# Optimization experiments

Hardware: AMD Instinct MI355X
Metric: run time of the kernel (lower is better)

The kernel has to match this reference:

```python
import jax, jax.numpy as jnp
import numpy as np

K = 20
EPS = 1e-5
N = 4096


def lrelu(x):
    return jnp.where(x >= 0, x, 0.2 * x)


def bn(x, g, b, m, v):
    # eval-mode BatchNorm over channel dim 1
    shape = [1] * x.ndim
    shape[1] = -1
    inv = g / jnp.sqrt(v + EPS)
    return (x - m.reshape(shape)) * inv.reshape(shape) + b.reshape(shape)


def get_graph_feature(x):
    # Faithful to repo: num_points = x.shape[1], remaining dims fold into channels.
    p = x.shape[1]
    x2d = x.reshape(-1, p)              # (C, P)
    xx = jnp.sum(x2d * x2d, axis=0)     # (P,)
    dist = 2.0 * (x2d.T @ x2d) - xx[:, None] - xx[None, :]  # -||xi-xj||^2, (P, P)
    idx = jax.lax.top_k(dist, K)[1]     # (P, K) nearest neighbors (incl. self)
    xt = x2d.T                          # (P, C)
    feat = xt[idx]                      # (P, K, C) neighbor gather
    ctr = jnp.broadcast_to(xt[:, None, :], feat.shape)
    out = jnp.concatenate([feat - ctr, ctr], axis=-1)  # (P, K, 2C)
    return out.transpose(2, 0, 1)[None]                # (1, 2C, P, K)


def setup_inputs():
    key = jax.random.key(0)
    ks = jax.random.split(key, 16)

    def w(k_, o, c):
        return jax.random.normal(k_, (o, c), jnp.float32) / float(np.sqrt(c))

    def bnp(k_, c):
        k1, k2, k3, k4 = jax.random.split(k_, 4)
        return (1.0 + 0.1 * jax.random.normal(k1, (c,), jnp.float32),
                0.1 * jax.random.normal(k2, (c,), jnp.float32),
                0.1 * jax.random.normal(k3, (c,), jnp.float32),
                jax.random.uniform(k4, (c,), jnp.float32, minval=0.5, maxval=1.5))

    g1, b1, m1, v1 = bnp(ks[1], 64)
    g2, b2, m2, v2 = bnp(ks[2], 64)
    g3, b3, m3, v3 = bnp(ks[3], 128)
    g4, b4, m4, v4 = bnp(ks[4], 256)
    g5, b5, m5, v5 = bnp(ks[5], 512)
    return dict(
        x=jax.random.normal(ks[0], (3, N), jnp.float32),
        w1=w(ks[6], 64, 6), g1=g1, b1=b1, m1=m1, v1=v1,
        w2=w(ks[7], 64, 64), g2=g2, b2=b2, m2=m2, v2=v2,
        w3=w(ks[8], 128, 64), g3=g3, b3=b3, m3=m3, v3=v3,
        w4=w(ks[9], 256, 128), g4=g4, b4=b4, m4=m4, v4=v4,
        w5=w(ks[10], 512, 256), g5=g5, b5=b5, m5=m5, v5=v5,
        lw1=w(ks[11], 512, 1024),
        lw2=w(ks[12], 256, 512),
        lb2=0.1 * jax.random.normal(ks[13], (256,), jnp.float32),
        ow=w(ks[14], 11, 256),
        ob=0.1 * jax.random.normal(ks[15], (11,), jnp.float32),
    )


def reference(x, w1, g1, b1, m1, v1, w2, g2, b2, m2, v2, w3, g3, b3, m3, v3,
              w4, g4, b4, m4, v4, w5, g5, b5, m5, v5, lw1, lw2, lb2, ow, ob):
    conv2d = lambda w_, f_: jnp.einsum('oc,bcpk->bopk', w_, f_)

    f = get_graph_feature(x)                                   # (1, 6, N, K)
    h = lrelu(bn(conv2d(w1, f), g1, b1, m1, v1))
    x1 = jnp.max(h, axis=-1)                                   # (1, 64, N)

    f = jnp.swapaxes(get_graph_feature(x1), 1, 2)              # (1, 64, 2N, K)
    h = lrelu(bn(conv2d(w2, f), g2, b2, m2, v2))
    x2 = jnp.max(h, axis=-1)                                   # (1, 64, 2N)

    f = jnp.swapaxes(get_graph_feature(x2), 1, 2)              # (1, 64, 4N, K)
    h = lrelu(bn(conv2d(w3, f), g3, b3, m3, v3))
    x3 = jnp.max(h, axis=-1)                                   # (1, 128, 4N)

    f = jnp.swapaxes(get_graph_feature(x3), 1, 2)              # (1, 128, 8N, K)
    h = lrelu(bn(conv2d(w4, f), g4, b4, m4, v4))
    x4 = jnp.max(h, axis=-1)                                   # (1, 256, 8N)

    h5 = lrelu(bn(jnp.einsum('oc,bcp->bop', w5, x4), g5, b5, m5, v5))  # (1, 512, 8N)
    pmax = jnp.max(h5, axis=-1)
    pavg = jnp.mean(h5, axis=-1)
    z = jnp.concatenate([pmax, pavg], axis=1)                  # (1, 1024)
    z = lrelu(z @ lw1.T)                                       # (1, 512); dropout = eval identity
    z = lrelu(z @ lw2.T + lb2)                                 # (1, 256)
    logits = z @ ow.T + ob                                     # (1, 11)
    return jax.nn.softmax(logits, axis=1)
```

## Files before the change

kernel.cpp:

```cpp
#include <hip/hip_runtime.h>
#include <hip/hip_bf16.h>
#include <float.h>
#include <math.h>

#define DEV __device__ __forceinline__

DEV float lrelu(float x) { return x >= 0.f ? x : 0.2f * x; }

constexpr int N = 4096, KNN = 20;

typedef __attribute__((ext_vector_type(4))) float f32x4;
typedef __attribute__((ext_vector_type(8))) short s16x8;

constexpr size_t OFF_SC1 = 0,    OFF_SH1 = 64;
constexpr size_t OFF_SC2 = 128,  OFF_SH2 = 192;
constexpr size_t OFF_SC3 = 256,  OFF_SH3 = 384;
constexpr size_t OFF_SC4 = 512,  OFF_SH4 = 768;
constexpr size_t OFF_SC5 = 1024, OFF_SH5 = 1536;
constexpr size_t OFF_X1 = 2048;
constexpr size_t OFF_X2 = OFF_X1 + (size_t)64*4096;
constexpr size_t OFF_X3 = OFF_X2 + (size_t)64*8192;
constexpr size_t OFF_X4 = OFF_X3 + (size_t)128*16384;
constexpr size_t OFF_A  = OFF_X4 + (size_t)256*32768;
constexpr size_t OFF_GP = OFF_A + (size_t)256*21*128;
constexpr size_t OFF_PM = OFF_GP + (size_t)64*128*128;
constexpr size_t OFF_PS = OFF_PM + (size_t)512*256;
constexpr size_t OFF_Z0 = OFF_PS + (size_t)512*256;
constexpr size_t OFF_Z1 = OFF_Z0 + 1024;
constexpr size_t OFF_Z2 = OFF_Z1 + 512;
constexpr size_t OFF_IDX = OFF_Z2 + 256;
constexpr size_t WS_NEEDED_BYTES = OFF_IDX * 4 + (size_t)N * KNN * 4;
constexpr size_t OFF_ABF = OFF_A;
constexpr size_t OFF_W5BF = OFF_A + 524288;

__global__ void k_ws_sentinel(float* out, float mb) {
  int t = threadIdx.x;
  if (t < 11) out[t] = 1.0e6f + mb;
}

__global__ __launch_bounds__(512) void k_bn_pre(
    const float* g1, const float* b1, const float* m1, const float* v1,
    const float* g2, const float* b2, const float* m2, const float* v2,
    const float* g3, const float* b3, const float* m3, const float* v3,
    const float* g4, const float* b4, const float* m4, const float* v4,
    const float* g5, const float* b5, const float* m5, const float* v5,
    float* ws) {
  int t = threadIdx.x;
  const float* G[5] = {g1,g2,g3,g4,g5};
  const float* B[5] = {b1,b2,b3,b4,b5};
  const float* M[5] = {m1,m2,m3,m4,m5};
  const float* V[5] = {v1,v2,v3,v4,v5};
  const size_t SC[5] = {OFF_SC1,OFF_SC2,OFF_SC3,OFF_SC4,OFF_SC5};
  const size_t SH[5] = {OFF_SH1,OFF_SH2,OFF_SH3,OFF_SH4,OFF_SH5};
  const int CN[5] = {64,64,128,256,512};
  for (int s = 0; s < 5; ++s) {
    for (int i = t; i < CN[s]; i += 512) {
      float scale = G[s][i] / sqrtf(V[s][i] + 1e-5f);
      ws[SC[s] + i] = scale;
      ws[SH[s] + i] = B[s][i] - M[s][i] * scale;
    }
  }
}

__global__ __launch_bounds__(256, 4) void k_s1_topk(const float* x, int* idx) {
  int t = threadIdx.x;
  int lane = t & 63, wid = t >> 6;
  int i = blockIdx.x*4 + wid;
  float v[64];
  {
    #pragma clang fp contract(off)
    float xi0 = x[i], xi1 = x[N + i], xi2 = x[2*N + i];
    float sqi = xi0*xi0 + xi1*xi1 + xi2*xi2;
    #pragma unroll
    for (int u = 0; u < 64; ++u) {
      int j = u*64 + lane;
      float xj0 = x[j], xj1 = x[N+j], xj2 = x[2*N+j];
      float sqj = xj0*xj0 + xj1*xj1 + xj2*xj2;
      float p = xi0*xj0 + xi1*xj1 + xi2*xj2;
      v[u] = (2.f*p - sqi) - sqj;
    }
  }
  float bv = -FLT_MAX; int bi = N;
  #pragma unroll
  for (int u = 0; u < 64; ++u) {
    int j = u*64 + lane;
    if (v[u] > bv) { bv = v[u]; bi = j; }
  }
  for (int k = 0; k < KNN; ++k) {
    float rv = bv; int ri = bi;
    #pragma unroll
    for (int off = 1; off < 64; off <<= 1) {
      float v2 = __shfl_xor(rv, off); int i2 = __shfl_xor(ri, off);
      if (v2 > rv || (v2 == rv && i2 < ri)) { rv = v2; ri = i2; }
    }
    if (lane == 0) idx[i*KNN + k] = ri;
    if ((ri & 63) == lane) {
      int wu = ri >> 6;
      bv = -FLT_MAX; bi = N;
      #pragma unroll
      for (int u = 0; u < 64; ++u) {
        if (u == wu) v[u] = -FLT_MAX;
        int j = u*64 + lane;
        if (v[u] > bv) { bv = v[u]; bi = j; }
      }
    }
  }
}

__global__ __launch_bounds__(256) void k_s1_conv(const float* x, const float* w1g,
                                                 const int* idx, const float* sc, const float* sh, float* x1) {
  __shared__ int idxs[64][KNN];
  __shared__ float xs[3][64];
  __shared__ float wsh[4][6];
  int t = threadIdx.x, bx = blockIdx.x, by = blockIdx.y;
  int i0 = bx * 64;
  for (int u = t; u < 64*KNN; u += 256) idxs[u/KNN][u%KNN] = idx[(size_t)(i0 + u/KNN)*KNN + u%KNN];
  for (int u = t; u < 3*64; u += 256) xs[u/64][u%64] = x[(size_t)(u/64)*N + i0 + (u%64)];
  for (int u = t; u < 24; u += 256) wsh[u/6][u%6] = w1g[(size_t)(by*4 + u/6)*6 + u%6];
  __syncthreads();
  int il = t & 63, ol = t >> 6;
  int o = by*4 + ol, i = i0 + il;
  float xi0 = xs[0][il], xi1 = xs[1][il], xi2 = xs[2][il];
  float w0 = wsh[ol][0], w1v = wsh[ol][1], w2v = wsh[ol][2];
  float w3v = wsh[ol][3], w4v = wsh[ol][4], w5v = wsh[ol][5];
  float ctr = w3v*xi0 + w4v*xi1 + w5v*xi2;
  float scale = sc[o], shift = sh[o];
  float best = -FLT_MAX;
  for (int k = 0; k < KNN; ++k) {
    int j = idxs[il][k];
    float h = w0*(x[j] - xi0) + w1v*(x[N+j] - xi1) + w2v*(x[2*N+j] - xi2) + ctr;
    h = lrelu(h*scale + shift);
    best = fmaxf(best, h);
  }
  x1[(size_t)o*N + i] = best;
}

template<int P>
__global__ __launch_bounds__(256) void k_gram_partial(const float* prev, int C, float* gp) {
  constexpr int BI = P / 16;
  __shared__ float ysh[32][P];
  int b = blockIdx.x, t = threadIdx.x;
  int R = C / gridDim.x;
  int base = b * R;
  float acc[BI][BI] = {};
  int i0 = (t >> 4) * BI, j0 = (t & 15) * BI;
  for (int r0 = 0; r0 < R; r0 += 32) {
    for (int u = t; u < 32*P; u += 256) ysh[u/P][u%P] = prev[(size_t)(base + r0 + u/P)*P + (u%P)];
    __syncthreads();
    for (int r = 0; r < 32; ++r) {
      float yi[BI], yj[BI];
      #pragma unroll
      for (int a = 0; a < BI; ++a) { yi[a] = ysh[r][i0+a]; yj[a] = ysh[r][j0+a]; }
      #pragma unroll
      for (int a = 0; a < BI; ++a)
        #pragma unroll
        for (int c = 0; c < BI; ++c) acc[a][c] += yi[a]*yj[c];
    }
    __syncthreads();
  }
  for (int a = 0; a < BI; ++a)
    for (int c = 0; c < BI; ++c)
      gp[(size_t)b*P*P + (size_t)(i0+a)*P + (j0+c)] = acc[a][c];
}

template<int P>
__global__ __launch_bounds__(128) void k_dist_topk(const float* gp, int* idx, int nb) {
  __shared__ float dsh[P];
  __shared__ float diag[P];
  __shared__ float vsh[128];
  __shared__ int ish[128];
  int i = blockIdx.x, t = threadIdx.x;
  if (t < P) {
    int q = nb >> 2;
    float g0 = 0.f, g1 = 0.f, g2 = 0.f, g3 = 0.f;
    float e0 = 0.f, e1 = 0.f, e2 = 0.f, e3 = 0.f;
    for (int b = 0; b < q; ++b) {
      size_t o0 = (size_t)b*P*P, o1 = (size_t)(b+q)*P*P, o2 = (size_t)(b+2*q)*P*P, o3 = (size_t)(b+3*q)*P*P;
      g0 += gp[o0 + (size_t)i*P + t]; g1 += gp[o1 + (size_t)i*P + t];
      g2 += gp[o2 + (size_t)i*P + t]; g3 += gp[o3 + (size_t)i*P + t];
      e0 += gp[o0 + (size_t)t*P + t]; e1 += gp[o1 + (size_t)t*P + t];
      e2 += gp[o2 + (size_t)t*P + t]; e3 += gp[o3 + (size_t)t*P + t];
    }
    diag[t] = (e0 + e1) + (e2 + e3);
    dsh[t] = (g0 + g1) + (g2 + g3);
  }
  __syncthreads();
  if (t < P) dsh[t] = (2.f*dsh[t] - diag[i]) - diag[t];
  __syncthreads();
  for (int k = 0; k < KNN; ++k) {
    float bv = -FLT_MAX; int bi = P;
    if (t < P) { bv = dsh[t]; bi = t; }
    vsh[t] = bv; ish[t] = bi;
    __syncthreads();
    for (int s = 64; s > 0; s >>= 1) {
      if (t < s) {
        float v2 = vsh[t+s]; int i2 = ish[t+s];
        if (v2 > vsh[t] || (v2 == vsh[t] && i2 < ish[t])) { vsh[t] = v2; ish[t] = i2; }
      }
      __syncthreads();
    }
    if (t == 0) { idx[i*KNN + k] = ish[0]; dsh[ish[0]] = -FLT_MAX; }
    __syncthreads();
  }
}

template<int P>
__global__ __launch_bounds__(64) void k_build_A(const float* w, const int* idx, int O, float* A) {
  __shared__ float row[64][P];
  int t = threadIdx.x;
  int r = blockIdx.x*64 + t;
  if (r < O*21) {
    int o = r / 21, kk = r % 21;
    float* my = row[t];
    if (kk == 20) {
      for (int i2 = 0; i2 < P; ++i2) my[i2] = w[(size_t)o*P + i2];
    } else {
      for (int i2 = 0; i2 < P; ++i2) my[i2] = 0.f;
      for (int j = 0; j < P; ++j) my[idx[j*KNN + kk]] += w[(size_t)o*P + j];
    }
    for (int i2 = 0; i2 < P; ++i2) A[(size_t)r*P + i2] = my[i2];
  }
}

__global__ __launch_bounds__(64) void k_build_A_bf(const float* w, const int* idx, __hip_bfloat16* A) {
  __shared__ float row[64][128];
  int t = threadIdx.x;
  int r = blockIdx.x*64 + t;
  int o = r >> 5, kk = r & 31;
  float* my = row[t];
  if (kk == 20) {
    for (int i2 = 0; i2 < 128; ++i2) my[i2] = w[(size_t)o*128 + i2];
  } else if (kk < 20) {
    for (int i2 = 0; i2 < 128; ++i2) my[i2] = 0.f;
    for (int j = 0; j < 128; ++j) my[idx[j*KNN + kk]] += w[(size_t)o*128 + j];
  } else {
    for (int i2 = 0; i2 < 128; ++i2) my[i2] = 0.f;
  }
  for (int i2 = 0; i2 < 128; ++i2) A[(size_t)r*128 + i2] = __float2bfloat16(my[i2]);
}

__global__ __launch_bounds__(256) void k_f32_to_bf16(const float* in, __hip_bfloat16* out) {
  size_t base = ((size_t)blockIdx.x*256 + threadIdx.x) * 16;
  #pragma unroll
  for (int j = 0; j < 4; ++j) {
    float4 v = *(const float4*)(in + base + j*4);
    __hip_bfloat16 tmp[4] = {__float2bfloat16(v.x), __float2bfloat16(v.y),
                             __float2bfloat16(v.z), __float2bfloat16(v.w)};
    *(ushort4*)(out + base + j*4) = *(const ushort4*)tmp;
  }
}

__global__ __launch_bounds__(512, 2) void k_conv4_mfma(const __hip_bfloat16* Abf, const __hip_bfloat16* Xbf,
                                                       const float* sc, const float* sh, float* x4) {
  constexpr int MT = 256;
  __shared__ char Bs[MT*256];
  int t = threadIdx.x, bx = blockIdx.x, byg = blockIdx.y;
  int m0 = bx*MT;
  for (int u = t; u < MT*16; u += 512) {
    int row = u >> 4, k8 = u & 15;
    s16x8 v = *(const s16x8*)(Xbf + ((size_t)(m0+row) << 7) + (k8 << 3));
    *(s16x8*)(Bs + (row << 8) + ((k8 << 4) ^ ((row & 7) << 4))) = v;
  }
  __syncthreads();
  int lane = t & 63, w = t >> 6;
  int col = lane & 15, lg = lane >> 4;
  int q = w & 3, pb = w >> 2;
  for (int it = 0; it < 8; ++it) {
    int by = byg*16 + it*2 + pb;
    const __hip_bfloat16* Ab = Abf + ((size_t)(by*64) << 7);
    f32x4 acc[4][4] = {};
    #pragma unroll
    for (int ks = 0; ks < 4; ++ks) {
      int kel = ks*32 + lg*8;
      int kbyte = ks*64 + lg*16;
      s16x8 a[4], b[4];
      #pragma unroll
      for (int at = 0; at < 4; ++at)
        a[at] = *(const s16x8*)(Ab + ((size_t)(at*16 + col) << 7) + kel);
      #pragma unroll
      for (int bt = 0; bt < 4; ++bt) {
        int r = q*64 + bt*16 + col;
        b[bt] = *(const s16x8*)(Bs + (r << 8) + (kbyte ^ ((r & 7) << 4)));
      }
      #pragma unroll
      for (int at = 0; at < 4; ++at)
        #pragma unroll
        for (int bt = 0; bt < 4; ++bt)
          acc[at][bt] = __builtin_amdgcn_mfma_f32_16x16x32_bf16(a[at], b[bt], acc[at][bt], 0, 0, 0);
    }
    int o0 = by*2;
    #pragma unroll
    for (int ol = 0; ol < 2; ++ol) {
      float scale = sc[o0+ol], shift = sh[o0+ol];
      float mxv[4], ctv[4];
      #pragma unroll
      for (int bt = 0; bt < 4; ++bt) {
        float h2b = __shfl(acc[2*ol+1][bt][0], 16 + col);
        float mx = -FLT_MAX;
        #pragma unroll
        for (int qq = 0; qq < 4; ++qq) {
          mx = fmaxf(mx, lrelu((acc[2*ol][bt][qq] - h2b)*scale + shift));
          float v1 = lrelu((acc[2*ol+1][bt][qq] - h2b)*scale + shift);
          if (lg == 0) mx = fmaxf(mx, v1);
        }
        mx = fmaxf(mx, __shfl_xor(mx, 16));
        mx = fmaxf(mx, __shfl_xor(mx, 32));
        mxv[bt] = mx;
        ctv[bt] = lrelu(h2b*scale + shift);
      }
      float vb = (lg == 0) ? mxv[0] : (lg == 1) ? mxv[1] : (lg == 2) ? mxv[2] : mxv[3];
      float vc = (lg == 0) ? ctv[0] : (lg == 1) ? ctv[1] : (lg == 2) ? ctv[2] : ctv[3];
      size_t pbase = (size_t)(o0+ol)*32768 + m0 + q*64 + lane;
      x4[pbase] = vb;
      x4[pbase + 16384] = vc;
    }
  }
}

template<int P>
__global__ __launch_bounds__(256) void k_fused_conv(const float* prev, const float* A,
                                                    const float* sc, const float* sh,
                                                    int C, float* outx) {
  constexpr int TO = 8, ROWS = TO*21;
  __shared__ float Ash[ROWS][65];
  __shared__ float Bsh[64][132];
  int bx = blockIdx.x, by = blockIdx.y, t = threadIdx.x;
  int m0 = bx*128;
  int rowbase = by*ROWS;
  int ol = t >> 5, mg = t & 31;
  float acc[21][4] = {};
  for (int ic = 0; ic < P/64; ++ic) {
    for (int u = t; u < ROWS*64; u += 256) {
      int rr = u >> 6, cc = u & 63;
      Ash[rr][cc] = A[(size_t)(rowbase + rr)*P + ic*64 + cc];
    }
    for (int u = t; u < 64*128; u += 256) {
      int mr = u >> 6, ii = u & 63;
      Bsh[ii][mr] = prev[(size_t)(m0 + mr)*P + ic*64 + ii];
    }
    __syncthreads();
    for (int i = 0; i < 64; ++i) {
      float v0 = Bsh[i][mg*4+0], v1 = Bsh[i][mg*4+1], v2 = Bsh[i][mg*4+2], v3 = Bsh[i][mg*4+3];
      #pragma unroll
      for (int kk = 0; kk < 21; ++kk) {
        float a = Ash[ol*21 + kk][i];
        acc[kk][0] += a*v0; acc[kk][1] += a*v1; acc[kk][2] += a*v2; acc[kk][3] += a*v3;
      }
    }
    __syncthreads();
  }
  int o = by*TO + ol;
  float scale = sc[o], shift = sh[o];
  size_t C2 = 2*(size_t)C;
  #pragma unroll
  for (int mm = 0; mm < 4; ++mm) {
    int m = m0 + mg*4 + mm;
    float h2 = acc[20][mm];
    float ctr = lrelu(h2*scale + shift);
    float best = -FLT_MAX;
    #pragma unroll
    for (int kk = 0; kk < 20; ++kk) {
      float v = lrelu((acc[kk][mm] - h2)*scale + shift);
      best = fmaxf(best, v);
    }
    outx[(size_t)o*C2 + m] = best;
    outx[(size_t)o*C2 + C + m] = ctr;
  }
}

__global__ __launch_bounds__(256) void k_s5_mfma(const float* x4, const __hip_bfloat16* w5bf,
                                                 const float* sc, const float* sh,
                                                 float* pm, float* ps) {
  __shared__ char smem[8192 + 32768];
  __shared__ float redm[64][4];
  __shared__ float reds[64][4];
  int t = threadIdx.x, bx = blockIdx.x, by = blockIdx.y;
  int p0 = bx*256, o0 = by*64;
  int lane = t & 63, w = t >> 6;
  int lrow = lane & 15, lg = lane >> 4;
  char* As = smem;
  char* Bs = smem + 8192;
  f32x4 acc[4][4] = {};
  for (int c0 = 0; c0 < 256; c0 += 64) {
    for (int u = t; u < 64*8; u += 256) {
      int row = u >> 3, k8 = u & 7;
      s16x8 v = *(const s16x8*)(w5bf + (size_t)(o0+row)*256 + c0 + k8*8);
      *(s16x8*)(As + row*128 + ((k8*16) ^ ((row&7)<<4))) = v;
    }
    #pragma unroll
    for (int i = 0; i < 8; ++i) {
      __hip_bfloat16 tmp[8];
      #pragma unroll
      for (int j = 0; j < 8; ++j)
        tmp[j] = __float2bfloat16(x4[(size_t)(c0 + i*8 + j)*32768 + p0 + t]);
      *(s16x8*)(Bs + t*128 + ((i*16) ^ ((t&7)<<4))) = *(const s16x8*)tmp;
    }
    __syncthreads();
    #pragma unroll
    for (int ksub = 0; ksub < 2; ++ksub) {
      int kbyte = ksub*64 + lg*16;
      s16x8 a[4], b[4];
      #pragma unroll
      for (int rt = 0; rt < 4; ++rt) { int r = rt*16 + lrow; a[rt] = *(const s16x8*)(As + r*128 + (kbyte ^ ((r&7)<<4))); }
      #pragma unroll
      for (int cf = 0; cf < 4; ++cf) { int r = w*64 + cf*16 + lrow; b[cf] = *(const s16x8*)(Bs + r*128 + (kbyte ^ ((r&7)<<4))); }
      #pragma unroll
      for (int rt = 0; rt < 4; ++rt)
        #pragma unroll
        for (int cf = 0; cf < 4; ++cf)
          acc[rt][cf] = __builtin_amdgcn_mfma_f32_16x16x32_bf16(a[rt], b[cf], acc[rt][cf], 0, 0, 0);
    }
    __syncthreads();
  }
  #pragma unroll
  for (int rt = 0; rt < 4; ++rt) {
    #pragma unroll
    for (int q = 0; q < 4; ++q) {
      int ol = rt*16 + lg*4 + q;
      float scale = sc[o0+ol], shift = sh[o0+ol];
      float mx = -FLT_MAX, sm = 0.f;
      #pragma unroll
      for (int cf = 0; cf < 4; ++cf) {
        float h = lrelu(acc[rt][cf][q]*scale + shift);
        mx = fmaxf(mx, h); sm += h;
      }
      #pragma unroll
      for (int off2 = 1; off2 < 16; off2 <<= 1) {
        mx = fmaxf(mx, __shfl_xor(mx, off2));
        sm += __shfl_xor(sm, off2);
      }
      if (lrow == 0) { redm[ol][w] = mx; reds[ol][w] = sm; }
    }
  }
  __syncthreads();
  if (t < 64) {
    float mx = fmaxf(fmaxf(redm[t][0], redm[t][1]), fmaxf(redm[t][2], redm[t][3]));
    float sm = reds[t][0] + reds[t][1] + reds[t][2] + reds[t][3];
    pm[(size_t)(o0 + t)*128 + bx] = mx;
    ps[(size_t)(o0 + t)*128 + bx] = sm;
  }
}

__global__ __launch_bounds__(512) void k_pool(const float* pm, const float* ps, float* z0) {
  int t = threadIdx.x;
  for (int o = t; o < 512; o += 512) {
    float mx = -FLT_MAX, sm = 0.f;
    for (int nt = 0; nt < 128; ++nt) { mx = fmaxf(mx, pm[(size_t)o*128+nt]); sm += ps[(size_t)o*128+nt]; }
    z0[o] = mx;
    z0[512+o] = sm * (1.f/32768.f);
  }
}

__global__ __launch_bounds__(128) void k_fc1(const float* z0, const float* lw1, float* z1) {
  int bx = blockIdx.x, t = threadIdx.x;
  int rl = t >> 4, cl = t & 15;
  int r = bx*8 + rl;
  float acc = 0.f;
  for (int u = 0; u < 64; ++u) {
    int c = cl*64 + u;
    acc += z0[c] * lw1[(size_t)r*1024 + c];
  }
  #pragma unroll
  for (int off = 1; off < 16; off <<= 1) acc += __shfl_xor(acc, off);
  if (cl == 0) z1[r] = lrelu(acc);
}

__global__ __launch_bounds__(128) void k_fc2(const float* z1, const float* lw2,
                                             const float* lb2, float* z2) {
  int bx = blockIdx.x, t = threadIdx.x;
  int rl = t >> 4, cl = t & 15;
  int r = bx*8 + rl;
  float acc = 0.f;
  for (int u = 0; u < 32; ++u) {
    int c = cl*32 + u;
    acc += z1[c] * lw2[(size_t)r*512 + c];
  }
  #pragma unroll
  for (int off = 1; off < 16; off <<= 1) acc += __shfl_xor(acc, off);
  if (cl == 0) z2[r] = lrelu(acc + lb2[r]);
}

__global__ __launch_bounds__(64) void k_fc3(const float* z2, const float* ow,
                                            const float* ob, float* out) {
  __shared__ float lg[11];
  __shared__ float ex[11];
  int t = threadIdx.x;
  if (t < 11) {
    float acc = 0.f;
    for (int c = 0; c < 256; ++c) acc += z2[c] * ow[t*256 + c];
    lg[t] = acc + ob[t];
  }
  __syncthreads();
  if (t < 11) {
    float m = -FLT_MAX;
    for (int r = 0; r < 11; ++r) m = fmaxf(m, lg[r]);
    ex[t] = expf(lg[t] - m);
  }
  __syncthreads();
  if (t < 11) {
    float s = 0.f;
    for (int r = 0; r < 11; ++r) s += ex[r];
    out[t] = ex[t] / s;
  }
}

extern "C" void kernel_launch(void* const* d_in, const int* in_sizes, int n_in,
                              void* d_out, int out_size, void* d_ws, size_t ws_size,
                              hipStream_t stream) {
  auto f = [&](int i) { return (const float*)d_in[i]; };
  float* ws = (float*)d_ws;
  int* idx = (int*)(ws + OFF_IDX);
  float* out = (float*)d_out;

  if (ws_size < WS_NEEDED_BYTES) {
    k_ws_sentinel<<<1, 64, 0, stream>>>(out, (float)(ws_size >> 20));
    return;
  }

  __hip_bfloat16* Abf = (__hip_bfloat16*)(ws + OFF_ABF);
  __hip_bfloat16* Xbf = (__hip_bfloat16*)(ws + OFF_GP);
  __hip_bfloat16* w5bf = (__hip_bfloat16*)(ws + OFF_W5BF);
  float* x4 = ws + OFF_X4;

  k_bn_pre<<<1, 512, 0, stream>>>(f(2),f(3),f(4),f(5), f(7),f(8),f(9),f(10),
                                  f(12),f(13),f(14),f(15), f(17),f(18),f(19),f(20),
                                  f(22),f(23),f(24),f(25), ws);
  k_s1_topk<<<N/4, 256, 0, stream>>>(f(0), idx);
  k_s1_conv<<<dim3(N/64, 16), 256, 0, stream>>>(f(0), f(1), idx, ws+OFF_SC1, ws+OFF_SH1, ws+OFF_X1);
  k_gram_partial<64><<<64, 256, 0, stream>>>(ws+OFF_X1, 4096, ws+OFF_GP);
  k_dist_topk<64><<<64, 128, 0, stream>>>(ws+OFF_GP, idx, 64);
  k_build_A<64><<<21, 64, 0, stream>>>(f(6), idx, 64, ws+OFF_A);
  k_fused_conv<64><<<dim3(4096/128, 64/8), 256, 0, stream>>>(ws+OFF_X1, ws+OFF_A, ws+OFF_SC2, ws+OFF_SH2, 4096, ws+OFF_X2);
  k_gram_partial<64><<<64, 256, 0, stream>>>(ws+OFF_X2, 8192, ws+OFF_GP);
  k_dist_topk<64><<<64, 128, 0, stream>>>(ws+OFF_GP, idx, 64);
  k_build_A<64><<<42, 64, 0, stream>>>(f(11), idx, 128, ws+OFF_A);
  k_fused_conv<64><<<dim3(8192/128, 128/8), 256, 0, stream>>>(ws+OFF_X2, ws+OFF_A, ws+OFF_SC3, ws+OFF_SH3, 8192, ws+OFF_X3);
  k_gram_partial<128><<<64, 256, 0, stream>>>(ws+OFF_X3, 16384, ws+OFF_GP);
  k_dist_topk<128><<<128, 128, 0, stream>>>(ws+OFF_GP, idx, 64);
  k_build_A_bf<<<128, 64, 0, stream>>>(f(16), idx, Abf);
  k_f32_to_bf16<<<512, 256, 0, stream>>>(ws+OFF_X3, Xbf);
  k_conv4_mfma<<<dim3(16384/256, 8), 512, 0, stream>>>(Abf, Xbf, ws+OFF_SC4, ws+OFF_SH4, x4);
  k_f32_to_bf16<<<32, 256, 0, stream>>>(f(21), w5bf);
  k_s5_mfma<<<dim3(128, 8), 256, 0, stream>>>(x4, w5bf, ws+OFF_SC5, ws+OFF_SH5, ws+OFF_PM, ws+OFF_PS);
  k_pool<<<1, 512, 0, stream>>>(ws+OFF_PM, ws+OFF_PS, ws+OFF_Z0);
  k_fc1<<<64, 128, 0, stream>>>(ws+OFF_Z0, f(26), ws+OFF_Z1);
  k_fc2<<<32, 128, 0, stream>>>(ws+OFF_Z1, f(27), f(28), ws+OFF_Z2);
  k_fc3<<<1, 64, 0, stream>>>(ws+OFF_Z2, f(29), f(30), out);
}
```

Measured before the change: 507.0 us.

## Move stage 2/3 fused conv to split-bf16 MFMA with three-product error compensation

Replaces the scalar fp32 fused conv kernels for stages 2 and 3 with an MFMA kernel. Both the neighbour-folded weight matrix and the point features are split into bf16 hi and lo parts, and hi*hi + hi*lo + lo*hi are accumulated to keep near-fp32 accuracy. This is meant to cut the FMA-bound scalar GEMM time, at the cost of extra split kernels and three times the MFMA work.

New measurement: 487.7 us. 3.8% less time.

```diff
diff --git a/kernel.cpp b/kernel.cpp
--- a/kernel.cpp
+++ b/kernel.cpp
@@ -32,6 +32,7 @@
 constexpr size_t WS_NEEDED_BYTES = OFF_IDX * 4 + (size_t)N * KNN * 4;
 constexpr size_t OFF_ABF = OFF_A;
 constexpr size_t OFF_W5BF = OFF_A + 524288;
+constexpr size_t OFF_SPLIT = OFF_GP + 524288;
 
 __global__ void k_ws_sentinel(float* out, float mb) {
   int t = threadIdx.x;
@@ -204,21 +205,26 @@
   }
 }
 
-template<int P>
-__global__ __launch_bounds__(64) void k_build_A(const float* w, const int* idx, int O, float* A) {
-  __shared__ float row[64][P];
+__global__ __launch_bounds__(64) void k_build_A_bf32(const float* w, const int* idx,
+                                                     __hip_bfloat16* Ah, __hip_bfloat16* Al) {
+  __shared__ float row[64][64];
   int t = threadIdx.x;
   int r = blockIdx.x*64 + t;
-  if (r < O*21) {
-    int o = r / 21, kk = r % 21;
-    float* my = row[t];
-    if (kk == 20) {
-      for (int i2 = 0; i2 < P; ++i2) my[i2] = w[(size_t)o*P + i2];
-    } else {
-      for (int i2 = 0; i2 < P; ++i2) my[i2] = 0.f;
-      for (int j = 0; j < P; ++j) my[idx[j*KNN + kk]] += w[(size_t)o*P + j];
-    }
-    for (int i2 = 0; i2 < P; ++i2) A[(size_t)r*P + i2] = my[i2];
+  int o = r >> 5, kk = r & 31;
+  float* my = row[t];
+  if (kk == 20) {
+    for (int i2 = 0; i2 < 64; ++i2) my[i2] = w[(size_t)o*64 + i2];
+  } else if (kk < 20) {
+    for (int i2 = 0; i2 < 64; ++i2) my[i2] = 0.f;
+    for (int j = 0; j < 64; ++j) my[idx[j*KNN + kk]] += w[(size_t)o*64 + j];
+  } else {
+    for (int i2 = 0; i2 < 64; ++i2) my[i2] = 0.f;
+  }
+  for (int i2 = 0; i2 < 64; ++i2) {
+    float v = my[i2];
+    __hip_bfloat16 h = __float2bfloat16(v);
+    Ah[(size_t)r*64 + i2] = h;
+    Al[(size_t)r*64 + i2] = __float2bfloat16(v - (float)h);
   }
 }
 
@@ -250,48 +256,79 @@
   }
 }
 
-__global__ __launch_bounds__(512, 2) void k_conv4_mfma(const __hip_bfloat16* Abf, const __hip_bfloat16* Xbf,
-                                                       const float* sc, const float* sh, float* x4) {
-  constexpr int MT = 256;
-  __shared__ char Bs[MT*256];
+__global__ __launch_bounds__(256) void k_split_bf16x2(const float* in, __hip_bfloat16* hi, __hip_bfloat16* lo) {
+  size_t base = ((size_t)blockIdx.x*256 + threadIdx.x) * 4;
+  float4 v = *(const float4*)(in + base);
+  float a[4] = {v.x, v.y, v.z, v.w};
+  __hip_bfloat16 h[4], l[4];
+  #pragma unroll
+  for (int j = 0; j < 4; ++j) {
+    h[j] = __float2bfloat16(a[j]);
+    l[j] = __float2bfloat16(a[j] - (float)h[j]);
+  }
+  *(ushort4*)(hi + base) = *(const ushort4*)h;
+  *(ushort4*)(lo + base) = *(const ushort4*)l;
+}
+
+__global__ __launch_bounds__(512, 2) void k_fconv_mfma(const __hip_bfloat16* Ah, const __hip_bfloat16* Al,
+                                                       const __hip_bfloat16* Bh, const __hip_bfloat16* Bl,
+                                                       const float* sc, const float* sh,
+                                                       int C, int nit, float* outx) {
+  __shared__ char Bs[65536];
+  __shared__ float scl[16], shl[16];
   int t = threadIdx.x, bx = blockIdx.x, byg = blockIdx.y;
-  int m0 = bx*MT;
-  for (int u = t; u < MT*16; u += 512) {
-    int row = u >> 4, k8 = u & 15;
-    s16x8 v = *(const s16x8*)(Xbf + ((size_t)(m0+row) << 7) + (k8 << 3));
-    *(s16x8*)(Bs + (row << 8) + ((k8 << 4) ^ ((row & 7) << 4))) = v;
-  }
+  int m0 = bx*256;
+  for (int u = t; u < 256*8; u += 512) {
+    int row = u >> 3, k8 = u & 7;
+    s16x8 v = *(const s16x8*)(Bh + (size_t)(m0+row)*64 + k8*8);
+    *(s16x8*)(Bs + row*128 + ((k8*16) ^ ((row&7)<<4))) = v;
+  }
+  for (int u = t; u < 256*8; u += 512) {
+    int row = u >> 3, k8 = u & 7;
+    s16x8 v = *(const s16x8*)(Bl + (size_t)(m0+row)*64 + k8*8);
+    *(s16x8*)(Bs + 32768 + row*128 + ((k8*16) ^ ((row&7)<<4))) = v;
+  }
+  int obase = byg*4*nit;
+  if (t < 4*nit) { scl[t] = sc[obase + t]; shl[t] = sh[obase + t]; }
   __syncthreads();
   int lane = t & 63, w = t >> 6;
   int col = lane & 15, lg = lane >> 4;
   int q = w & 3, pb = w >> 2;
-  for (int it = 0; it < 8; ++it) {
-    int by = byg*16 + it*2 + pb;
-    const __hip_bfloat16* Ab = Abf + ((size_t)(by*64) << 7);
+  for (int it = 0; it < nit; ++it) {
+    int by = byg*2*nit + it*2 + pb;
+    int rb = by*64;
     f32x4 acc[4][4] = {};
     #pragma unroll
-    for (int ks = 0; ks < 4; ++ks) {
+    for (int ks = 0; ks < 2; ++ks) {
       int kel = ks*32 + lg*8;
       int kbyte = ks*64 + lg*16;
-      s16x8 a[4], b[4];
-      #pragma unroll
-      for (int at = 0; at < 4; ++at)
-        a[at] = *(const s16x8*)(Ab + ((size_t)(at*16 + col) << 7) + kel);
+      s16x8 ah[4], al[4], bh[4], bl[4];
+      #pragma unroll
+      for (int at = 0; at < 4; ++at) {
+        int r = rb + at*16 + col;
+        ah[at] = *(const s16x8*)(Ah + (size_t)r*64 + kel);
+        al[at] = *(const s16x8*)(Al + (size_t)r*64 + kel);
+      }
       #pragma unroll
       for (int bt = 0; bt < 4; ++bt) {
         int r = q*64 + bt*16 + col;
-        b[bt] = *(const s16x8*)(Bs + (r << 8) + (kbyte ^ ((r & 7) << 4)));
+        int off = r*128 + (kbyte ^ ((r & 7) << 4));
+        bh[bt] = *(const s16x8*)(Bs + off);
+        bl[bt] = *(const s16x8*)(Bs + 32768 + off);
       }
       #pragma unroll
       for (int at = 0; at < 4; ++at)
         #pragma unroll
-        for (int bt = 0; bt < 4; ++bt)
-          acc[at][bt] = __builtin_amdgcn_mfma_f32_16x16x32_bf16(a[at], b[bt], acc[at][bt], 0, 0, 0);
+        for (int bt = 0; bt < 4; ++bt) {
+          acc[at][bt] = __builtin_amdgcn_mfma_f32_16x16x32_bf16(al[at], bh[bt], acc[at][bt], 0, 0, 0);
+          acc[at][bt] = __builtin_amdgcn_mfma_f32_16x16x32_bf16(ah[at], bl[bt], acc[at][bt], 0, 0, 0);
+          acc[at][bt] = __builtin_amdgcn_mfma_f32_16x16x32_bf16(ah[at], bh[bt], acc[at][bt], 0, 0, 0);
+        }
     }
     int o0 = by*2;
     #pragma unroll
     for (int ol = 0; ol < 2; ++ol) {
-      float scale = sc[o0+ol], shift = sh[o0+ol];
+      float scale = scl[o0 + ol - obase], shift = shl[o0 + ol - obase];
       float mxv[4], ctv[4];
       #pragma unroll
       for (int bt = 0; bt < 4; ++bt) {
@@ -310,61 +347,77 @@
       }
       float vb = (lg == 0) ? mxv[0] : (lg == 1) ? mxv[1] : (lg == 2) ? mxv[2] : mxv[3];
       float vc = (lg == 0) ? ctv[0] : (lg == 1) ? ctv[1] : (lg == 2) ? ctv[2] : ctv[3];
+      size_t pbase = (size_t)(o0+ol)*2*C + m0 + q*64 + lane;
+      outx[pbase] = vb;
+      outx[pbase + C] = vc;
+    }
+  }
+}
+
+__global__ __launch_bounds__(512, 2) void k_conv4_mfma(const __hip_bfloat16* Abf, const __hip_bfloat16* Xbf,
+                                                       const float* sc, const float* sh, float* x4) {
+  constexpr int MT = 256;
+  __shared__ char Bs[MT*256];
+  int t = threadIdx.x, bx = blockIdx.x, byg = blockIdx.y;
+  int m0 = bx*MT;
+  for (int u = t; u < MT*16; u += 512) {
+    int row = u >> 4, k8 = u & 15;
+    s16x8 v = *(const s16x8*)(Xbf + ((size_t)(m0+row) << 7) + (k8 << 3));
+    *(s16x8*)(Bs + (row << 8) + ((k8 << 4) ^ ((row & 7) << 4))) = v;
+  }
+  __syncthreads();
+  int lane = t & 63, w = t >> 6;
+  int col = lane & 15, lg = lane >> 4;
+  int q = w & 3, pb = w >> 2;
+  for (int it = 0; it < 8; ++it) {
+    int by = byg*16 + it*2 + pb;
+    const __hip_bfloat16* Ab = Abf + ((size_t)(by*64) << 7);
+    f32x4 acc[4][4] = {};
+    #pragma unroll
+    for (int ks = 0; ks < 4; ++ks) {
+      int kel = ks*32 + lg*8;
+      int kbyte = ks*64 + lg*16;
+      s16x8 a[4], b[4];
+      #pragma unroll
+      for (int at = 0; at < 4; ++at)
+        a[at] = *(const s16x8*)(Ab + ((size_t)(at*16 + col) << 7) + kel);
+      #pragma unroll
+      for (int bt = 0; bt < 4; ++bt) {
+        int r = q*64 + bt*16 + col;
+        b[bt] = *(const s16x8*)(Bs + (r << 8) + (kbyte ^ ((r & 7) << 4)));
+      }
+      #pragma unroll
+      for (int at = 0; at < 4; ++at)
+        #pragma unroll
+        for (int bt = 0; bt < 4; ++bt)
+          acc[at][bt] = __builtin_amdgcn_mfma_f32_16x16x32_bf16(a[at], b[bt], acc[at][bt], 0, 0, 0);
+    }
+    int o0 = by*2;
+    #pragma unroll
+    for (int ol = 0; ol < 2; ++ol) {
+      float scale = sc[o0+ol], shift = sh[o0+ol];
+      float mxv[4], ctv[4];
+      #pragma unroll
+      for (int bt = 0; bt < 4; ++bt) {
+        float h2b = __shfl(acc[2*ol+1][bt][0], 16 + col);
+        float mx = -FLT_MAX;
+        #pragma unroll
+        for (int qq = 0; qq < 4; ++qq) {
+          mx = fmaxf(mx, lrelu((acc[2*ol][bt][qq] - h2b)*scale + shift));
+          float v1 = lrelu((acc[2*ol+1][bt][qq] - h2b)*scale + shift);
+          if (lg == 0) mx = fmaxf(mx, v1);
+        }
+        mx = fmaxf(mx, __shfl_xor(mx, 16));
+        mx = fmaxf(mx, __shfl_xor(mx, 32));
+        mxv[bt] = mx;
+        ctv[bt] = lrelu(h2b*scale + shift);
+      }
+      float vb = (lg == 0) ? mxv[0] : (lg == 1) ? mxv[1] : (lg == 2) ? mxv[2] : mxv[3];
+      float vc = (lg == 0) ? ctv[0] : (lg == 1) ? ctv[1] : (lg == 2) ? ctv[2] : ctv[3];
       size_t pbase = (size_t)(o0+ol)*32768 + m0 + q*64 + lane;
       x4[pbase] = vb;
       x4[pbase + 16384] = vc;
     }
-  }
-}
-
-template<int P>
-__global__ __launch_bounds__(256) void k_fused_conv(const float* prev, const float* A,
-                                                    const float* sc, const float* sh,
-                                                    int C, float* outx) {
-  constexpr int TO = 8, ROWS = TO*21;
-  __shared__ float Ash[ROWS][65];
-  __shared__ float Bsh[64][132];
-  int bx = blockIdx.x, by = blockIdx.y, t = threadIdx.x;
-  int m0 = bx*128;
-  int rowbase = by*ROWS;
-  int ol = t >> 5, mg = t & 31;
-  float acc[21][4] = {};
-  for (int ic = 0; ic < P/64; ++ic) {
-    for (int u = t; u < ROWS*64; u += 256) {
-      int rr = u >> 6, cc = u & 63;
-      Ash[rr][cc] = A[(size_t)(rowbase + rr)*P + ic*64 + cc];
-    }
-    for (int u = t; u < 64*128; u += 256) {
-      int mr = u >> 6, ii = u & 63;
-      Bsh[ii][mr] = prev[(size_t)(m0 + mr)*P + ic*64 + ii];
-    }
-    __syncthreads();
-    for (int i = 0; i < 64; ++i) {
-      float v0 = Bsh[i][mg*4+0], v1 = Bsh[i][mg*4+1], v2 = Bsh[i][mg*4+2], v3 = Bsh[i][mg*4+3];
-      #pragma unroll
-      for (int kk = 0; kk < 21; ++kk) {
-        float a = Ash[ol*21 + kk][i];
-        acc[kk][0] += a*v0; acc[kk][1] += a*v1; acc[kk][2] += a*v2; acc[kk][3] += a*v3;
-      }
-    }
-    __syncthreads();
-  }
-  int o = by*TO + ol;
-  float scale = sc[o], shift = sh[o];
-  size_t C2 = 2*(size_t)C;
-  #pragma unroll
-  for (int mm = 0; mm < 4; ++mm) {
-    int m = m0 + mg*4 + mm;
-    float h2 = acc[20][mm];
-    float ctr = lrelu(h2*scale + shift);
-    float best = -FLT_MAX;
-    #pragma unroll
-    for (int kk = 0; kk < 20; ++kk) {
-      float v = lrelu((acc[kk][mm] - h2)*scale + shift);
-      best = fmaxf(best, v);
-    }
-    outx[(size_t)o*C2 + m] = best;
-    outx[(size_t)o*C2 + C + m] = ctr;
   }
 }
 
@@ -521,6 +574,13 @@
   __hip_bfloat16* Xbf = (__hip_bfloat16*)(ws + OFF_GP);
   __hip_bfloat16* w5bf = (__hip_bfloat16*)(ws + OFF_W5BF);
   float* x4 = ws + OFF_X4;
+  __hip_bfloat16* Xh = (__hip_bfloat16*)(ws + OFF_SPLIT);
+  __hip_bfloat16* X1L = Xh + 262144;
+  __hip_bfloat16* X2L = Xh + 524288;
+  __hip_bfloat16* A2H = (__hip_bfloat16*)(ws + OFF_A);
+  __hip_bfloat16* A2L = A2H + 131072;
+  __hip_bfloat16* A3H = (__hip_bfloat16*)(ws + OFF_A);
+  __hip_bfloat16* A3L = A3H + 262144;
 
   k_bn_pre<<<1, 512, 0, stream>>>(f(2),f(3),f(4),f(5), f(7),f(8),f(9),f(10),
                                   f(12),f(13),f(14),f(15), f(17),f(18),f(19),f(20),
@@ -529,12 +589,14 @@
   k_s1_conv<<<dim3(N/64, 16), 256, 0, stream>>>(f(0), f(1), idx, ws+OFF_SC1, ws+OFF_SH1, ws+OFF_X1);
   k_gram_partial<64><<<64, 256, 0, stream>>>(ws+OFF_X1, 4096, ws+OFF_GP);
   k_dist_topk<64><<<64, 128, 0, stream>>>(ws+OFF_GP, idx, 64);
-  k_build_A<64><<<21, 64, 0, stream>>>(f(6), idx, 64, ws+OFF_A);
-  k_fused_conv<64><<<dim3(4096/128, 64/8), 256, 0, stream>>>(ws+OFF_X1, ws+OFF_A, ws+OFF_SC2, ws+OFF_SH2, 4096, ws+OFF_X2);
+  k_build_A_bf32<<<32, 64, 0, stream>>>(f(6), idx, A2H, A2L);
+  k_split_bf16x2<<<256, 256, 0, stream>>>(ws+OFF_X1, Xh, X1L);
+  k_fconv_mfma<<<dim3(16, 8), 512, 0, stream>>>(A2H, A2L, Xh, X1L, ws+OFF_SC2, ws+OFF_SH2, 4096, 2, ws+OFF_X2);
   k_gram_partial<64><<<64, 256, 0, stream>>>(ws+OFF_X2, 8192, ws+OFF_GP);
   k_dist_topk<64><<<64, 128, 0, stream>>>(ws+OFF_GP, idx, 64);
-  k_build_A<64><<<42, 64, 0, stream>>>(f(11), idx, 128, ws+OFF_A);
-  k_fused_conv<64><<<dim3(8192/128, 128/8), 256, 0, stream>>>(ws+OFF_X2, ws+OFF_A, ws+OFF_SC3, ws+OFF_SH3, 8192, ws+OFF_X3);
+  k_build_A_bf32<<<64, 64, 0, stream>>>(f(11), idx, A3H, A3L);
+  k_split_bf16x2<<<512, 256, 0, stream>>>(ws+OFF_X2, Xh, X2L);
+  k_fconv_mfma<<<dim3(32, 8), 512, 0, stream>>>(A3H, A3L, Xh, X2L, ws+OFF_SC3, ws+OFF_SH3, 8192, 4, ws+OFF_X3);
   k_gram_partial<128><<<64, 256, 0, stream>>>(ws+OFF_X3, 16384, ws+OFF_GP);
   k_dist_topk<128><<<128, 128, 0, stream>>>(ws+OFF_GP, idx, 64);
   k_build_A_bf<<<128, 64, 0, stream>>>(f(16), idx, Abf);
```
